# Performance work log

Hardware: AMD Instinct MI355X
Metric: run time of the kernel (lower is better)

Reference implementation:

```python
import jax, jax.numpy as jnp
import numpy as np

B, SQ, ST, SI = 8, 4096, 77, 16
C, DC, H = 1280, 2048, 20
DH = C // H  # 64
SCALE = 1.0 / np.sqrt(DH).astype(np.float32)
SCALE_ID = 1.0
SCALE_HAIR = 1.0


def setup_inputs() -> dict:
    key = jax.random.key(0)
    ks = jax.random.split(key, 12)
    std = 0.02
    return {
        "hidden_states": jax.random.normal(ks[0], (B, SQ, C), jnp.float32),
        "text_states": jax.random.normal(ks[1], (B, ST, DC), jnp.float32),
        "id_states": jax.random.normal(ks[2], (B, SI, DC), jnp.float32),
        "hair_states": jax.random.normal(ks[3], (B, SI, DC), jnp.float32),
        # weights stored as [in, out] (transpose of torch nn.Linear layout)
        "Wq": jax.random.normal(ks[4], (C, C), jnp.float32) * std,
        "Wk": jax.random.normal(ks[5], (DC, C), jnp.float32) * std,
        "Wv": jax.random.normal(ks[6], (DC, C), jnp.float32) * std,
        "Wo": jax.random.normal(ks[7], (C, C), jnp.float32) * std,
        "b_o": jnp.zeros((C,), jnp.float32),
        "Wk_id": jax.random.normal(ks[8], (DC, C), jnp.float32) * std,
        "Wv_id": jax.random.normal(ks[9], (DC, C), jnp.float32) * std,
        "Wk_hair": jax.random.normal(ks[10], (DC, C), jnp.float32) * std,
        "Wv_hair": jax.random.normal(ks[11], (DC, C), jnp.float32) * std,
    }


def _heads(x):
    # [B, S, C] -> [B, H, S, DH]
    b, s, _ = x.shape
    return x.reshape(b, s, H, DH).transpose(0, 2, 1, 3)


def _merge(x):
    # [B, H, S, DH] -> [B, S, C]
    b, h, s, d = x.shape
    return x.transpose(0, 2, 1, 3).reshape(b, s, h * d)


def _attend(q, k, v):
    # q: [B,H,Sq,DH], k/v: [B,H,Sk,DH]; fp32 scores (attn_fp32=True)
    scores = jnp.einsum("bhqd,bhkd->bhqk", q.astype(jnp.float32), k.astype(jnp.float32)) * SCALE
    p = jax.nn.softmax(scores, axis=-1)
    return jnp.einsum("bhqk,bhkd->bhqd", p, v.astype(jnp.float32))


def reference(hidden_states, text_states, id_states, hair_states, Wq, Wk, Wv, Wo, b_o, Wk_id, Wv_id, Wk_hair, Wv_hair):
    q = _heads(hidden_states @ Wq)
    # base cross-attention to text (standard diffusers AttnProcessor)
    base = _attend(q, _heads(text_states @ Wk), _heads(text_states @ Wv))
    result = _merge(base) @ Wo + b_o
    # ID branch: own K/V projections, shared query and to_out
    out_id = _attend(q, _heads(id_states @ Wk_id), _heads(id_states @ Wv_id))
    result = result + SCALE_ID * (_merge(out_id) @ Wo + b_o)
    # hair branch
    out_h = _attend(q, _heads(hair_states @ Wk_hair), _heads(hair_states @ Wv_hair))
    result = result + SCALE_HAIR * (_merge(out_h) @ Wo + b_o)
    return result
```

## Files before the change

### kernel.cpp

```cpp
#include <hip/hip_runtime.h>
#include <cstdint>
#include <cstddef>

typedef unsigned short u16;
typedef __attribute__((ext_vector_type(4))) float     f32x4_t;
typedef __attribute__((ext_vector_type(8))) __bf16    bf16x8_t;
typedef __attribute__((ext_vector_type(8))) u16       u16x8_t;
typedef __attribute__((ext_vector_type(4))) u16       u16x4_t;
typedef __attribute__((ext_vector_type(4))) float     fvec4_t;

#define DEVI __device__ __forceinline__

constexpr int Bn  = 8;
constexpr int SQn = 4096;
constexpr int STn = 77;
constexpr int SIn = 16;
constexpr int Cn  = 1280;
constexpr int DCn = 2048;
constexpr int Hn  = 20;
constexpr float SCALEf = 0.125f;
constexpr float L2E    = 1.4426950408889634f;

typedef const __attribute__((address_space(1))) void* gas_t;
typedef __attribute__((address_space(3))) void*       las_t;

DEVI u16 f2bf(float f) {
  union { float f; unsigned u; } cv; cv.f = f;
  unsigned u = cv.u;
  return (u16)((u + 0x7FFFu + ((u >> 16) & 1u)) >> 16);
}

__global__ __launch_bounds__(256) void cast_bf16_kernel(
    const float* __restrict__ src, u16* __restrict__ dst, int n8) {
  int i = blockIdx.x * 256 + threadIdx.x;
  if (i >= n8) return;
  const fvec4_t* s4 = (const fvec4_t*)src;
  fvec4_t a = s4[2 * i], b = s4[2 * i + 1];
  u16x8_t o;
  o[0] = f2bf(a[0]); o[1] = f2bf(a[1]); o[2] = f2bf(a[2]); o[3] = f2bf(a[3]);
  o[4] = f2bf(b[0]); o[5] = f2bf(b[1]); o[6] = f2bf(b[2]); o[7] = f2bf(b[3]);
  ((u16x8_t*)dst)[i] = o;
}

struct TrArgs {
  const float* src[8];
  u16*         dst[8];
  int          Kd[8];
};

__global__ __launch_bounds__(256) void transpose_cast_kernel(TrArgs ta) {
  int z = blockIdx.z;
  int K = ta.Kd[z];
  int k0 = blockIdx.x * 32;
  if (k0 >= K) return;
  int n0 = blockIdx.y * 32;
  __shared__ float tile[32][33];
  int tx = threadIdx.x & 31, ty = threadIdx.x >> 5;
  const float* src = ta.src[z];
#pragma unroll
  for (int i = 0; i < 4; i++) {
    int r = ty + 8 * i;
    tile[r][tx] = src[(size_t)(k0 + r) * Cn + n0 + tx];
  }
  __syncthreads();
  u16* dst = ta.dst[z];
#pragma unroll
  for (int i = 0; i < 4; i++) {
    int r = ty + 8 * i;
    dst[(size_t)(n0 + r) * K + k0 + tx] = f2bf(tile[tx][r]);
  }
}

template <int OUT_MODE, int A_HM>
__global__ __launch_bounds__(512, 2) void gemm256_kernel(
    const u16* __restrict__ A, const u16* __restrict__ Bt,
    void* __restrict__ Cout, const float* __restrict__ bias, int M, int K) {
  __shared__ __align__(16) u16 lds[2][2][256 * 64];
  const int t = threadIdx.x;
  const int w = t >> 6, l = t & 63;
  const int wr = w >> 2, wc = w & 3;
  const int lr = l & 15;
  const int m0 = blockIdx.x * 256, n0 = blockIdx.y * 256;
  const int NT = K >> 6;

  f32x4_t acc[8][4];
#pragma unroll
  for (int am = 0; am < 8; am++)
#pragma unroll
    for (int an = 0; an < 4; an++) {
      f32x4_t z = {0.f, 0.f, 0.f, 0.f};
      acc[am][an] = z;
    }

  auto stagePart = [&](int cb, int kt, int i) {
    const int k0 = kt * 64;
    int row = i * 64 + w * 8 + (l >> 3);
    int col16 = (l & 7) ^ (row & 7);
    const u16* ga;
    if (A_HM) {
      int gr = m0 + row, bb = gr >> 12, ss = gr & 4095;
      ga = A + (((size_t)bb * Hn + kt) * SQn + ss) * 64 + col16 * 8;
    } else {
      ga = A + (size_t)(m0 + row) * K + k0 + col16 * 8;
    }
    __builtin_amdgcn_global_load_lds((gas_t)ga, (las_t)(&lds[cb][0][0] + (size_t)(i * 512 + w * 64) * 8), 16, 0, 0);
    const u16* gb = Bt + (size_t)(n0 + row) * K + k0 + col16 * 8;
    __builtin_amdgcn_global_load_lds((gas_t)gb, (las_t)(&lds[cb][1][0] + (size_t)(i * 512 + w * 64) * 8), 16, 0, 0);
  };
  auto readA8 = [&](bf16x8_t (&dst)[8], const u16* bA, int kh) {
#pragma unroll
    for (int m = 0; m < 8; m++) {
      int row = wr * 128 + m * 16 + lr;
      int slot = kh * 4 + (l >> 4);
      dst[m] = *(const bf16x8_t*)&bA[row * 64 + ((slot ^ (row & 7)) * 8)];
    }
  };
  auto readB4 = [&](bf16x8_t (&dst)[4], const u16* bB, int kh) {
#pragma unroll
    for (int n = 0; n < 4; n++) {
      int row = wc * 64 + n * 16 + lr;
      int slot = kh * 4 + (l >> 4);
      dst[n] = *(const bf16x8_t*)&bB[row * 64 + ((slot ^ (row & 7)) * 8)];
    }
  };
  auto mfma32 = [&](bf16x8_t (&Af)[8], bf16x8_t (&Bf)[4]) {
    __builtin_amdgcn_s_setprio(1);
#pragma unroll
    for (int m = 0; m < 8; m++)
#pragma unroll
      for (int n = 0; n < 4; n++)
        acc[m][n] = __builtin_amdgcn_mfma_f32_16x16x32_bf16(Af[m], Bf[n], acc[m][n], 0, 0, 0);
    __builtin_amdgcn_s_setprio(0);
  };

#pragma unroll
  for (int i = 0; i < 4; i++) stagePart(0, 0, i);
#pragma unroll
  for (int i = 0; i < 4; i++) stagePart(1, 1, i);
  asm volatile("s_waitcnt vmcnt(8)" ::: "memory");
  __builtin_amdgcn_sched_barrier(0);
  __builtin_amdgcn_s_barrier();

  for (int kt = 0; kt < NT; kt++) {
    const int cb = kt & 1;
    const u16* bA = &lds[cb][0][0];
    const u16* bB = &lds[cb][1][0];
    const bool st = (kt + 2 < NT);
    bf16x8_t Af[8], Bf[4];

    readA8(Af, bA, 0);
    readB4(Bf, bB, 0);
    asm volatile("s_waitcnt lgkmcnt(0)" ::: "memory");
    __builtin_amdgcn_sched_barrier(0);
    mfma32(Af, Bf);

    readA8(Af, bA, 1);
    readB4(Bf, bB, 1);
    __builtin_amdgcn_s_barrier();
    if (st) {
      stagePart(cb, kt + 2, 0); stagePart(cb, kt + 2, 1);
      stagePart(cb, kt + 2, 2); stagePart(cb, kt + 2, 3);
    }
    asm volatile("s_waitcnt lgkmcnt(0)" ::: "memory");
    __builtin_amdgcn_sched_barrier(0);
    mfma32(Af, Bf);

    if (st) {
      asm volatile("s_waitcnt vmcnt(8)" ::: "memory");
    } else if (kt + 1 < NT) {
      asm volatile("s_waitcnt vmcnt(0)" ::: "memory");
    }
    __builtin_amdgcn_sched_barrier(0);
    __builtin_amdgcn_s_barrier();
  }

#pragma unroll
  for (int am = 0; am < 8; am++) {
    int rbase = m0 + wr * 128 + am * 16 + (l >> 4) * 4;
#pragma unroll
    for (int an = 0; an < 4; an++) {
      int col = n0 + wc * 64 + an * 16 + lr;
#pragma unroll
      for (int j = 0; j < 4; j++) {
        int r = rbase + j;
        if (OUT_MODE == 1) {
          ((float*)Cout)[(size_t)r * Cn + col] = acc[am][an][j] + 3.0f * bias[col];
        } else {
          int bb = r >> 12, ss = r & 4095;
          int hh = (n0 >> 6) + wc, dd = an * 16 + lr;
          ((u16*)Cout)[(((size_t)bb * Hn + hh) * SQn + ss) * 64 + dd] = f2bf(acc[am][an][j]);
        }
      }
    }
  }
}

DEVI void gemm_body(const u16* __restrict__ A, const u16* __restrict__ Bt,
                    u16* __restrict__ Cout, int M, int S, int K, int mtile, int ntile) {
  __shared__ __align__(16) u16 lA[128 * 64];
  __shared__ __align__(16) u16 lB[128 * 64];
  const int t = threadIdx.x;
  const int w = t >> 6, l = t & 63;
  const int wr = w >> 1, wc = w & 1;
  const int m0 = mtile * 128, n0 = ntile * 128;
  const int lr = l & 15, lk = (l >> 4) * 8;

  f32x4_t acc[4][4];
#pragma unroll
  for (int m = 0; m < 4; m++)
#pragma unroll
    for (int n = 0; n < 4; n++) {
      f32x4_t z = {0.f, 0.f, 0.f, 0.f};
      acc[m][n] = z;
    }

  for (int k0 = 0; k0 < K; k0 += 64) {
    __syncthreads();
#pragma unroll
    for (int i = 0; i < 4; i++) {
      int c = i * 256 + t;
      int row = c >> 3, ch = c & 7;
      int rA = m0 + row;
      rA = rA < M ? rA : M - 1;
      const u16* ga = A + (size_t)rA * K + k0 + ch * 8;
      __builtin_amdgcn_global_load_lds((gas_t)ga, (las_t)&lA[(i * 256 + w * 64) * 8], 16, 0, 0);
      const u16* gb = Bt + (size_t)(n0 + row) * K + k0 + ch * 8;
      __builtin_amdgcn_global_load_lds((gas_t)gb, (las_t)&lB[(i * 256 + w * 64) * 8], 16, 0, 0);
    }
    __syncthreads();
#pragma unroll
    for (int kk = 0; kk < 2; kk++) {
      bf16x8_t af[4], bf[4];
#pragma unroll
      for (int m = 0; m < 4; m++)
        af[m] = *(const bf16x8_t*)&lA[(64 * wr + 16 * m + lr) * 64 + kk * 32 + lk];
#pragma unroll
      for (int n = 0; n < 4; n++)
        bf[n] = *(const bf16x8_t*)&lB[(64 * wc + 16 * n + lr) * 64 + kk * 32 + lk];
#pragma unroll
      for (int m = 0; m < 4; m++)
#pragma unroll
        for (int n = 0; n < 4; n++)
          acc[m][n] = __builtin_amdgcn_mfma_f32_16x16x32_bf16(af[m], bf[n], acc[m][n], 0, 0, 0);
    }
  }

  const int rj = (l >> 4) * 4;
  const int hh = ntile * 2 + wc;
#pragma unroll
  for (int m = 0; m < 4; m++) {
    int rbase = m0 + 64 * wr + 16 * m + rj;
#pragma unroll
    for (int n = 0; n < 4; n++) {
      int dd = 16 * n + lr;
#pragma unroll
      for (int j = 0; j < 4; j++) {
        int r = rbase + j;
        if (r < M) {
          int bb = r / S, ss = r - bb * S;
          Cout[(((size_t)bb * Hn + hh) * S + ss) * 64 + dd] = f2bf(acc[m][n][j]);
        }
      }
    }
  }
}

struct KV6 {
  const u16* A[6];
  const u16* Bt[6];
  u16*       Cp[6];
  int        M[6];
  int        S[6];
};

__global__ __launch_bounds__(256) void gemm_kv_kernel(KV6 kv) {
  int z = blockIdx.z;
  int M = kv.M[z];
  if ((int)blockIdx.x * 128 >= M) return;
  gemm_body(kv.A[z], kv.Bt[z], kv.Cp[z], M, kv.S[z], DCn, blockIdx.x, blockIdx.y);
}

__global__ __launch_bounds__(256) void attn_kernel(
    const u16* __restrict__ q,
    const u16* __restrict__ ktx, const u16* __restrict__ vtx,
    const u16* __restrict__ kid, const u16* __restrict__ vid,
    const u16* __restrict__ kh,  const u16* __restrict__ vh,
    u16* __restrict__ osum) {
  __shared__ __align__(16) u16 KP[4 * 16 * 136];
  __shared__ __align__(16) u16 Vt[64 * 128];

  const int t = threadIdx.x, w = t >> 6, l = t & 63;
  const int bh = blockIdx.y;
  const int lr = l & 15, lk = (l >> 4) * 8;

  const u16* qB   = q   + ((size_t)bh) * SQn * 64;
  const u16* ktxB = ktx + ((size_t)bh) * STn * 64;
  const u16* vtxB = vtx + ((size_t)bh) * STn * 64;
  const u16* kidB = kid + ((size_t)bh) * SIn * 64;
  const u16* vidB = vid + ((size_t)bh) * SIn * 64;
  const u16* khB  = kh  + ((size_t)bh) * SIn * 64;
  const u16* vhB  = vh  + ((size_t)bh) * SIn * 64;
  u16*       oB   = osum + ((size_t)bh) * SQn * 64;

  for (int i = t; i < 112 * 8; i += 256) {
    int row = i >> 3, ch = i & 7;
    u16x8_t vv;
#pragma unroll
    for (int x = 0; x < 8; x++) vv[x] = 0;
    if (row < 77)
      vv = *(const u16x8_t*)(ktxB + (size_t)row * 64 + ch * 8);
    else if (row >= 80 && row < 96)
      vv = *(const u16x8_t*)(kidB + (size_t)(row - 80) * 64 + ch * 8);
    else if (row >= 96)
      vv = *(const u16x8_t*)(khB + (size_t)(row - 96) * 64 + ch * 8);
    *(u16x8_t*)&KP[row * 72 + ch * 8] = vv;
  }
  for (int i = t; i < 128 * 8; i += 256) {
    int key = i >> 3, ch = i & 7;
    u16x8_t vv;
#pragma unroll
    for (int x = 0; x < 8; x++) vv[x] = 0;
    if (key < 77)
      vv = *(const u16x8_t*)(vtxB + (size_t)key * 64 + ch * 8);
    else if (key >= 80 && key < 96)
      vv = *(const u16x8_t*)(vidB + (size_t)(key - 80) * 64 + ch * 8);
    else if (key >= 96 && key < 112)
      vv = *(const u16x8_t*)(vhB + (size_t)(key - 96) * 64 + ch * 8);
    int G = key >> 3, wk = key & 7;
#pragma unroll
    for (int x = 0; x < 8; x++) {
      int d = ch * 8 + x;
      int Gs = G ^ x ^ ch;
      Vt[d * 128 + Gs * 8 + wk] = vv[x];
    }
  }
  __syncthreads();

  bf16x8_t kf[7][2];
#pragma unroll
  for (int tt = 0; tt < 7; tt++)
#pragma unroll
    for (int kk = 0; kk < 2; kk++)
      kf[tt][kk] = *(const bf16x8_t*)&KP[(tt * 16 + lr) * 72 + kk * 32 + lk];
  __syncthreads();

  u16* Pw = &KP[w * 16 * 136];
  {
    u16x4_t z4; z4[0] = 0; z4[1] = 0; z4[2] = 0; z4[3] = 0;
    *(u16x4_t*)&Pw[(l >> 2) * 136 + 112 + (l & 3) * 4] = z4;
  }

  for (int rt = 0; rt < 4; rt++) {
    const int s0 = blockIdx.x * 256 + w * 64 + rt * 16;
    bf16x8_t qf[2];
#pragma unroll
    for (int kk = 0; kk < 2; kk++)
      qf[kk] = *(const bf16x8_t*)&qB[(size_t)(s0 + lr) * 64 + kk * 32 + lk];

    f32x4_t sc[7];
#pragma unroll
    for (int tt = 0; tt < 7; tt++) {
      f32x4_t z = {0.f, 0.f, 0.f, 0.f};
      z = __builtin_amdgcn_mfma_f32_16x16x32_bf16(qf[0], kf[tt][0], z, 0, 0, 0);
      z = __builtin_amdgcn_mfma_f32_16x16x32_bf16(qf[1], kf[tt][1], z, 0, 0, 0);
      sc[tt] = z;
    }
#pragma unroll
    for (int tt = 0; tt < 7; tt++)
#pragma unroll
      for (int j = 0; j < 4; j++) sc[tt][j] *= SCALEf;
    if (lr >= 13) {
#pragma unroll
      for (int j = 0; j < 4; j++) sc[4][j] = -3.0e38f;
    }

    float mx[4], sm[4], inv[4];

#pragma unroll
    for (int j = 0; j < 4; j++) {
      float m = sc[0][j];
      m = fmaxf(m, sc[1][j]); m = fmaxf(m, sc[2][j]);
      m = fmaxf(m, sc[3][j]); m = fmaxf(m, sc[4][j]);
      mx[j] = m;
    }
#pragma unroll
    for (int d = 1; d < 16; d <<= 1)
#pragma unroll
      for (int j = 0; j < 4; j++) mx[j] = fmaxf(mx[j], __shfl_xor(mx[j], d));
#pragma unroll
    for (int j = 0; j < 4; j++) sm[j] = 0.f;
#pragma unroll
    for (int tt = 0; tt < 5; tt++)
#pragma unroll
      for (int j = 0; j < 4; j++) {
        float p = __builtin_amdgcn_exp2f((sc[tt][j] - mx[j]) * L2E);
        sc[tt][j] = p;
        sm[j] += p;
      }
#pragma unroll
    for (int d = 1; d < 16; d <<= 1)
#pragma unroll
      for (int j = 0; j < 4; j++) sm[j] += __shfl_xor(sm[j], d);
#pragma unroll
    for (int j = 0; j < 4; j++) inv[j] = __builtin_amdgcn_rcpf(sm[j]);
#pragma unroll
    for (int tt = 0; tt < 5; tt++)
#pragma unroll
      for (int j = 0; j < 4; j++) {
        __bf16 pb = (__bf16)(sc[tt][j] * inv[j]);
        Pw[((l >> 4) * 4 + j) * 136 + tt * 16 + lr] = *(u16*)&pb;
      }

#pragma unroll
    for (int j = 0; j < 4; j++) mx[j] = sc[5][j];
#pragma unroll
    for (int d = 1; d < 16; d <<= 1)
#pragma unroll
      for (int j = 0; j < 4; j++) mx[j] = fmaxf(mx[j], __shfl_xor(mx[j], d));
#pragma unroll
    for (int j = 0; j < 4; j++) {
      float p = __builtin_amdgcn_exp2f((sc[5][j] - mx[j]) * L2E);
      sc[5][j] = p;
      sm[j] = p;
    }
#pragma unroll
    for (int d = 1; d < 16; d <<= 1)
#pragma unroll
      for (int j = 0; j < 4; j++) sm[j] += __shfl_xor(sm[j], d);
#pragma unroll
    for (int j = 0; j < 4; j++) {
      __bf16 pb = (__bf16)(sc[5][j] * __builtin_amdgcn_rcpf(sm[j]));
      Pw[((l >> 4) * 4 + j) * 136 + 80 + lr] = *(u16*)&pb;
    }

#pragma unroll
    for (int j = 0; j < 4; j++) mx[j] = sc[6][j];
#pragma unroll
    for (int d = 1; d < 16; d <<= 1)
#pragma unroll
      for (int j = 0; j < 4; j++) mx[j] = fmaxf(mx[j], __shfl_xor(mx[j], d));
#pragma unroll
    for (int j = 0; j < 4; j++) {
      float p = __builtin_amdgcn_exp2f((sc[6][j] - mx[j]) * L2E);
      sc[6][j] = p;
      sm[j] = p;
    }
#pragma unroll
    for (int d = 1; d < 16; d <<= 1)
#pragma unroll
      for (int j = 0; j < 4; j++) sm[j] += __shfl_xor(sm[j], d);
#pragma unroll
    for (int j = 0; j < 4; j++) {
      __bf16 pb = (__bf16)(sc[6][j] * __builtin_amdgcn_rcpf(sm[j]));
      Pw[((l >> 4) * 4 + j) * 136 + 96 + lr] = *(u16*)&pb;
    }

    f32x4_t oacc[4];
#pragma unroll
    for (int n = 0; n < 4; n++) {
      f32x4_t z = {0.f, 0.f, 0.f, 0.f};
      oacc[n] = z;
    }
#pragma unroll
    for (int ktile = 0; ktile < 4; ktile++) {
      bf16x8_t pf = *(const bf16x8_t*)&Pw[lr * 136 + ktile * 32 + lk];
#pragma unroll
      for (int n = 0; n < 4; n++) {
        int d = 16 * n + lr;
        int Gs = (4 * ktile + (l >> 4)) ^ (d & 7) ^ ((d >> 3) & 7);
        bf16x8_t vf = *(const bf16x8_t*)&Vt[d * 128 + Gs * 8];
        oacc[n] = __builtin_amdgcn_mfma_f32_16x16x32_bf16(pf, vf, oacc[n], 0, 0, 0);
      }
    }
#pragma unroll
    for (int n = 0; n < 4; n++)
#pragma unroll
      for (int j = 0; j < 4; j++) {
        int srow = s0 + (l >> 4) * 4 + j;
        __bf16 ob = (__bf16)oacc[n][j];
        oB[(size_t)srow * 64 + 16 * n + lr] = *(u16*)&ob;
      }
  }
}

extern "C" void kernel_launch(void* const* d_in, const int* in_sizes, int n_in,
                              void* d_out, int out_size, void* d_ws, size_t ws_size,
                              hipStream_t stream) {
  (void)in_sizes; (void)n_in; (void)out_size; (void)ws_size;
  const float* hidden  = (const float*)d_in[0];
  const float* text    = (const float*)d_in[1];
  const float* ids     = (const float*)d_in[2];
  const float* hair    = (const float*)d_in[3];
  const float* Wq      = (const float*)d_in[4];
  const float* Wk      = (const float*)d_in[5];
  const float* Wv      = (const float*)d_in[6];
  const float* Wo      = (const float*)d_in[7];
  const float* b_o     = (const float*)d_in[8];
  const float* Wk_id   = (const float*)d_in[9];
  const float* Wv_id   = (const float*)d_in[10];
  const float* Wk_hair = (const float*)d_in[11];
  const float* Wv_hair = (const float*)d_in[12];
  float* out = (float*)d_out;

  char* ws = (char*)d_ws;
  size_t off = 0;
  auto carve = [&](size_t bytes) -> char* {
    char* p = ws + off;
    off += (bytes + 255) & ~(size_t)255;
    return p;
  };

  u16* h_bf    = (u16*)carve((size_t)Bn * SQn * Cn * 2);
  u16* q_bf    = (u16*)carve((size_t)Bn * SQn * Cn * 2);
  u16* text_bf = (u16*)carve((size_t)Bn * STn * DCn * 2);
  u16* id_bf   = (u16*)carve((size_t)Bn * SIn * DCn * 2);
  u16* hair_bf = (u16*)carve((size_t)Bn * SIn * DCn * 2);
  u16* Wq_t    = (u16*)carve((size_t)Cn * Cn * 2);
  u16* Wo_t    = (u16*)carve((size_t)Cn * Cn * 2);
  u16* Wk_t    = (u16*)carve((size_t)DCn * Cn * 2);
  u16* Wv_t    = (u16*)carve((size_t)DCn * Cn * 2);
  u16* Wkid_t  = (u16*)carve((size_t)DCn * Cn * 2);
  u16* Wvid_t  = (u16*)carve((size_t)DCn * Cn * 2);
  u16* Wkh_t   = (u16*)carve((size_t)DCn * Cn * 2);
  u16* Wvh_t   = (u16*)carve((size_t)DCn * Cn * 2);
  u16* k_text  = (u16*)carve((size_t)Bn * STn * Cn * 2);
  u16* v_text  = (u16*)carve((size_t)Bn * STn * Cn * 2);
  u16* k_id    = (u16*)carve((size_t)Bn * SIn * Cn * 2);
  u16* v_id    = (u16*)carve((size_t)Bn * SIn * Cn * 2);
  u16* k_hr    = (u16*)carve((size_t)Bn * SIn * Cn * 2);
  u16* v_hr    = (u16*)carve((size_t)Bn * SIn * Cn * 2);
  u16* attn_sum = h_bf;

  {
    int n8 = Bn * SQn * Cn / 8;
    cast_bf16_kernel<<<dim3((n8 + 255) / 256), 256, 0, stream>>>(hidden, h_bf, n8);
  }
  {
    int n8 = Bn * STn * DCn / 8;
    cast_bf16_kernel<<<dim3((n8 + 255) / 256), 256, 0, stream>>>(text, text_bf, n8);
  }
  {
    int n8 = Bn * SIn * DCn / 8;
    cast_bf16_kernel<<<dim3((n8 + 255) / 256), 256, 0, stream>>>(ids, id_bf, n8);
    cast_bf16_kernel<<<dim3((n8 + 255) / 256), 256, 0, stream>>>(hair, hair_bf, n8);
  }

  {
    TrArgs ta;
    ta.src[0] = Wq;      ta.dst[0] = Wq_t;   ta.Kd[0] = Cn;
    ta.src[1] = Wo;      ta.dst[1] = Wo_t;   ta.Kd[1] = Cn;
    ta.src[2] = Wk;      ta.dst[2] = Wk_t;   ta.Kd[2] = DCn;
    ta.src[3] = Wv;      ta.dst[3] = Wv_t;   ta.Kd[3] = DCn;
    ta.src[4] = Wk_id;   ta.dst[4] = Wkid_t; ta.Kd[4] = DCn;
    ta.src[5] = Wv_id;   ta.dst[5] = Wvid_t; ta.Kd[5] = DCn;
    ta.src[6] = Wk_hair; ta.dst[6] = Wkh_t;  ta.Kd[6] = DCn;
    ta.src[7] = Wv_hair; ta.dst[7] = Wvh_t;  ta.Kd[7] = DCn;
    transpose_cast_kernel<<<dim3(DCn / 32, Cn / 32, 8), 256, 0, stream>>>(ta);
  }

  gemm256_kernel<2, 0><<<dim3(Bn * SQn / 256, Cn / 256), 512, 0, stream>>>(
      h_bf, Wq_t, q_bf, nullptr, Bn * SQn, Cn);

  {
    KV6 kv;
    kv.A[0] = text_bf; kv.Bt[0] = Wk_t;   kv.Cp[0] = k_text; kv.M[0] = Bn * STn; kv.S[0] = STn;
    kv.A[1] = text_bf; kv.Bt[1] = Wv_t;   kv.Cp[1] = v_text; kv.M[1] = Bn * STn; kv.S[1] = STn;
    kv.A[2] = id_bf;   kv.Bt[2] = Wkid_t; kv.Cp[2] = k_id;   kv.M[2] = Bn * SIn; kv.S[2] = SIn;
    kv.A[3] = id_bf;   kv.Bt[3] = Wvid_t; kv.Cp[3] = v_id;   kv.M[3] = Bn * SIn; kv.S[3] = SIn;
    kv.A[4] = hair_bf; kv.Bt[4] = Wkh_t;  kv.Cp[4] = k_hr;   kv.M[4] = Bn * SIn; kv.S[4] = SIn;
    kv.A[5] = hair_bf; kv.Bt[5] = Wvh_t;  kv.Cp[5] = v_hr;   kv.M[5] = Bn * SIn; kv.S[5] = SIn;
    gemm_kv_kernel<<<dim3((Bn * STn + 127) / 128, Cn / 128, 6), 256, 0, stream>>>(kv);
  }

  attn_kernel<<<dim3(SQn / 256, Bn * Hn), 256, 0, stream>>>(
      q_bf, k_text, v_text, k_id, v_id, k_hr, v_hr, attn_sum);

  gemm256_kernel<1, 1><<<dim3(Bn * SQn / 256, Cn / 256), 512, 0, stream>>>(
      attn_sum, Wo_t, out, b_o, Bn * SQn, Cn);
}
```

Baseline: 482.4 us.

## Software-pipeline LDS fragment reads with MFMAs and stage bf16 epilogue through LDS

The GEMM main loop now double-buffers the register fragments. The next half-K's LDS reads are issued before the current MFMA block, so LDS latency overlaps with matrix math instead of stalling before each MFMA group. For the head-major bf16 output mode, the epilogue writes accumulators into a padded, swizzled LDS region per wave and then emits 16-byte coalesced global stores, replacing scattered 2-byte writes. This raises LDS allocation for that mode and register pressure from holding two fragment sets, which could hurt occupancy at 2 blocks per CU.

Result: no change. 480.8 us (-0.3%).

```diff
diff --git a/kernel.cpp b/kernel.cpp
--- a/kernel.cpp
+++ b/kernel.cpp
@@ -75,7 +75,7 @@
 __global__ __launch_bounds__(512, 2) void gemm256_kernel(
     const u16* __restrict__ A, const u16* __restrict__ Bt,
     void* __restrict__ Cout, const float* __restrict__ bias, int M, int K) {
-  __shared__ __align__(16) u16 lds[2][2][256 * 64];
+  __shared__ __align__(16) u16 lds[(OUT_MODE == 2) ? 73728 : 65536];
   const int t = threadIdx.x;
   const int w = t >> 6, l = t & 63;
   const int wr = w >> 2, wc = w & 3;
@@ -83,6 +83,8 @@
   const int m0 = blockIdx.x * 256, n0 = blockIdx.y * 256;
   const int NT = K >> 6;
 
+  auto bufp = [&](int cb, int op) -> u16* { return lds + (size_t)(cb * 2 + op) * 16384; };
+
   f32x4_t acc[8][4];
 #pragma unroll
   for (int am = 0; am < 8; am++)
@@ -92,20 +94,23 @@
       acc[am][an] = z;
     }
 
-  auto stagePart = [&](int cb, int kt, int i) {
+  auto stageAll = [&](int cb, int kt) {
     const int k0 = kt * 64;
-    int row = i * 64 + w * 8 + (l >> 3);
-    int col16 = (l & 7) ^ (row & 7);
-    const u16* ga;
-    if (A_HM) {
-      int gr = m0 + row, bb = gr >> 12, ss = gr & 4095;
-      ga = A + (((size_t)bb * Hn + kt) * SQn + ss) * 64 + col16 * 8;
-    } else {
-      ga = A + (size_t)(m0 + row) * K + k0 + col16 * 8;
-    }
-    __builtin_amdgcn_global_load_lds((gas_t)ga, (las_t)(&lds[cb][0][0] + (size_t)(i * 512 + w * 64) * 8), 16, 0, 0);
-    const u16* gb = Bt + (size_t)(n0 + row) * K + k0 + col16 * 8;
-    __builtin_amdgcn_global_load_lds((gas_t)gb, (las_t)(&lds[cb][1][0] + (size_t)(i * 512 + w * 64) * 8), 16, 0, 0);
+#pragma unroll
+    for (int i = 0; i < 4; i++) {
+      int row = i * 64 + w * 8 + (l >> 3);
+      int col16 = (l & 7) ^ (row & 7);
+      const u16* ga;
+      if (A_HM) {
+        int gr = m0 + row, bb = gr >> 12, ss = gr & 4095;
+        ga = A + (((size_t)bb * Hn + kt) * SQn + ss) * 64 + col16 * 8;
+      } else {
+        ga = A + (size_t)(m0 + row) * K + k0 + col16 * 8;
+      }
+      __builtin_amdgcn_global_load_lds((gas_t)ga, (las_t)(bufp(cb, 0) + (size_t)(i * 512 + w * 64) * 8), 16, 0, 0);
+      const u16* gb = Bt + (size_t)(n0 + row) * K + k0 + col16 * 8;
+      __builtin_amdgcn_global_load_lds((gas_t)gb, (las_t)(bufp(cb, 1) + (size_t)(i * 512 + w * 64) * 8), 16, 0, 0);
+    }
   };
   auto readA8 = [&](bf16x8_t (&dst)[8], const u16* bA, int kh) {
 #pragma unroll
@@ -133,37 +138,30 @@
     __builtin_amdgcn_s_setprio(0);
   };
 
-#pragma unroll
-  for (int i = 0; i < 4; i++) stagePart(0, 0, i);
-#pragma unroll
-  for (int i = 0; i < 4; i++) stagePart(1, 1, i);
+  stageAll(0, 0);
+  stageAll(1, 1);
   asm volatile("s_waitcnt vmcnt(8)" ::: "memory");
   __builtin_amdgcn_sched_barrier(0);
   __builtin_amdgcn_s_barrier();
 
+  bf16x8_t Af0[8], Bf0[4], Af1[8], Bf1[4];
+  readA8(Af0, bufp(0, 0), 0);
+  readB4(Bf0, bufp(0, 1), 0);
+  asm volatile("s_waitcnt lgkmcnt(0)" ::: "memory");
+  __builtin_amdgcn_sched_barrier(0);
+
   for (int kt = 0; kt < NT; kt++) {
     const int cb = kt & 1;
-    const u16* bA = &lds[cb][0][0];
-    const u16* bB = &lds[cb][1][0];
     const bool st = (kt + 2 < NT);
-    bf16x8_t Af[8], Bf[4];
-
-    readA8(Af, bA, 0);
-    readB4(Bf, bB, 0);
+
+    readA8(Af1, bufp(cb, 0), 1);
+    readB4(Bf1, bufp(cb, 1), 1);
+    __builtin_amdgcn_sched_barrier(0);
+    __builtin_amdgcn_s_barrier();
+    if (st) stageAll(cb, kt + 2);
+    mfma32(Af0, Bf0);
     asm volatile("s_waitcnt lgkmcnt(0)" ::: "memory");
     __builtin_amdgcn_sched_barrier(0);
-    mfma32(Af, Bf);
-
-    readA8(Af, bA, 1);
-    readB4(Bf, bB, 1);
-    __builtin_amdgcn_s_barrier();
-    if (st) {
-      stagePart(cb, kt + 2, 0); stagePart(cb, kt + 2, 1);
-      stagePart(cb, kt + 2, 2); stagePart(cb, kt + 2, 3);
-    }
-    asm volatile("s_waitcnt lgkmcnt(0)" ::: "memory");
-    __builtin_amdgcn_sched_barrier(0);
-    mfma32(Af, Bf);
 
     if (st) {
       asm volatile("s_waitcnt vmcnt(8)" ::: "memory");
@@ -172,25 +170,57 @@
     }
     __builtin_amdgcn_sched_barrier(0);
     __builtin_amdgcn_s_barrier();
-  }
-
-#pragma unroll
-  for (int am = 0; am < 8; am++) {
-    int rbase = m0 + wr * 128 + am * 16 + (l >> 4) * 4;
-#pragma unroll
-    for (int an = 0; an < 4; an++) {
-      int col = n0 + wc * 64 + an * 16 + lr;
-#pragma unroll
-      for (int j = 0; j < 4; j++) {
-        int r = rbase + j;
-        if (OUT_MODE == 1) {
+
+    if (kt + 1 < NT) {
+      readA8(Af0, bufp(cb ^ 1, 0), 0);
+      readB4(Bf0, bufp(cb ^ 1, 1), 0);
+      __builtin_amdgcn_sched_barrier(0);
+    }
+    mfma32(Af1, Bf1);
+    asm volatile("s_waitcnt lgkmcnt(0)" ::: "memory");
+    __builtin_amdgcn_sched_barrier(0);
+  }
+
+  if (OUT_MODE == 1) {
+#pragma unroll
+    for (int am = 0; am < 8; am++) {
+      int rbase = m0 + wr * 128 + am * 16 + (l >> 4) * 4;
+#pragma unroll
+      for (int an = 0; an < 4; an++) {
+        int col = n0 + wc * 64 + an * 16 + lr;
+#pragma unroll
+        for (int j = 0; j < 4; j++) {
+          int r = rbase + j;
           ((float*)Cout)[(size_t)r * Cn + col] = acc[am][an][j] + 3.0f * bias[col];
-        } else {
-          int bb = r >> 12, ss = r & 4095;
-          int hh = (n0 >> 6) + wc, dd = an * 16 + lr;
-          ((u16*)Cout)[(((size_t)bb * Hn + hh) * SQn + ss) * 64 + dd] = f2bf(acc[am][an][j]);
         }
       }
+    }
+  } else {
+    __syncthreads();
+    u16* R = lds + (size_t)w * 9216;
+#pragma unroll
+    for (int am = 0; am < 8; am++)
+#pragma unroll
+      for (int an = 0; an < 4; an++)
+#pragma unroll
+        for (int j = 0; j < 4; j++) {
+          int row = am * 16 + (l >> 4) * 4 + j;
+          int g = an * 2 + (lr >> 3);
+          int gp = g ^ (row & 7);
+          R[row * 72 + gp * 8 + (lr & 7)] = f2bf(acc[am][an][j]);
+        }
+    const int hh = (n0 >> 6) + wc;
+    const int rbase = m0 + wr * 128;
+    const int bb = rbase >> 12;
+    const int ssb = rbase & 4095;
+    u16* dstW = (u16*)Cout + (((size_t)bb * Hn + hh) * SQn + ssb) * 64;
+#pragma unroll
+    for (int it = 0; it < 16; it++) {
+      int rr = it * 8 + (l >> 3);
+      int gr = l & 7;
+      int gp = gr ^ (rr & 7);
+      u16x8_t v = *(const u16x8_t*)&R[rr * 72 + gp * 8];
+      *(u16x8_t*)&dstW[(size_t)rr * 64 + gr * 8] = v;
     }
   }
 }
```

## Replace double-buffered LDS prefetch pipeline with single-buffer synchronous staging in GEMM

Applied to the files above, without the earlier changes.

Removes the two-stage LDS double buffering from the 256x256 GEMM kernel. Each K-tile is now loaded into a single LDS buffer, the kernel waits for all loads and synchronises, then computes. This halves LDS use per block, which may allow more resident blocks. In exchange, global-load latency is no longer overlapped with MFMA work inside a block.

Result: slower. 561.9 us (+16.5%).

```diff
diff --git a/kernel.cpp b/kernel.cpp
--- a/kernel.cpp
+++ b/kernel.cpp
@@ -75,7 +75,7 @@
 __global__ __launch_bounds__(512, 2) void gemm256_kernel(
     const u16* __restrict__ A, const u16* __restrict__ Bt,
     void* __restrict__ Cout, const float* __restrict__ bias, int M, int K) {
-  __shared__ __align__(16) u16 lds[2][2][256 * 64];
+  __shared__ __align__(16) u16 lds[2][256 * 64];
   const int t = threadIdx.x;
   const int w = t >> 6, l = t & 63;
   const int wr = w >> 2, wc = w & 3;
@@ -92,35 +92,38 @@
       acc[am][an] = z;
     }
 
-  auto stagePart = [&](int cb, int kt, int i) {
+  auto stageAll = [&](int kt) {
     const int k0 = kt * 64;
-    int row = i * 64 + w * 8 + (l >> 3);
-    int col16 = (l & 7) ^ (row & 7);
-    const u16* ga;
-    if (A_HM) {
-      int gr = m0 + row, bb = gr >> 12, ss = gr & 4095;
-      ga = A + (((size_t)bb * Hn + kt) * SQn + ss) * 64 + col16 * 8;
-    } else {
-      ga = A + (size_t)(m0 + row) * K + k0 + col16 * 8;
-    }
-    __builtin_amdgcn_global_load_lds((gas_t)ga, (las_t)(&lds[cb][0][0] + (size_t)(i * 512 + w * 64) * 8), 16, 0, 0);
-    const u16* gb = Bt + (size_t)(n0 + row) * K + k0 + col16 * 8;
-    __builtin_amdgcn_global_load_lds((gas_t)gb, (las_t)(&lds[cb][1][0] + (size_t)(i * 512 + w * 64) * 8), 16, 0, 0);
+#pragma unroll
+    for (int i = 0; i < 4; i++) {
+      int row = i * 64 + w * 8 + (l >> 3);
+      int col16 = (l & 7) ^ (row & 7);
+      const u16* ga;
+      if (A_HM) {
+        int gr = m0 + row, bb = gr >> 12, ss = gr & 4095;
+        ga = A + (((size_t)bb * Hn + kt) * SQn + ss) * 64 + col16 * 8;
+      } else {
+        ga = A + (size_t)(m0 + row) * K + k0 + col16 * 8;
+      }
+      __builtin_amdgcn_global_load_lds((gas_t)ga, (las_t)(&lds[0][0] + (size_t)(i * 512 + w * 64) * 8), 16, 0, 0);
+      const u16* gb = Bt + (size_t)(n0 + row) * K + k0 + col16 * 8;
+      __builtin_amdgcn_global_load_lds((gas_t)gb, (las_t)(&lds[1][0] + (size_t)(i * 512 + w * 64) * 8), 16, 0, 0);
+    }
   };
-  auto readA8 = [&](bf16x8_t (&dst)[8], const u16* bA, int kh) {
+  auto readA8 = [&](bf16x8_t (&dst)[8], int kh) {
 #pragma unroll
     for (int m = 0; m < 8; m++) {
       int row = wr * 128 + m * 16 + lr;
       int slot = kh * 4 + (l >> 4);
-      dst[m] = *(const bf16x8_t*)&bA[row * 64 + ((slot ^ (row & 7)) * 8)];
+      dst[m] = *(const bf16x8_t*)&lds[0][row * 64 + ((slot ^ (row & 7)) * 8)];
     }
   };
-  auto readB4 = [&](bf16x8_t (&dst)[4], const u16* bB, int kh) {
+  auto readB4 = [&](bf16x8_t (&dst)[4], int kh) {
 #pragma unroll
     for (int n = 0; n < 4; n++) {
       int row = wc * 64 + n * 16 + lr;
       int slot = kh * 4 + (l >> 4);
-      dst[n] = *(const bf16x8_t*)&bB[row * 64 + ((slot ^ (row & 7)) * 8)];
+      dst[n] = *(const bf16x8_t*)&lds[1][row * 64 + ((slot ^ (row & 7)) * 8)];
     }
   };
   auto mfma32 = [&](bf16x8_t (&Af)[8], bf16x8_t (&Bf)[4]) {
@@ -133,45 +136,24 @@
     __builtin_amdgcn_s_setprio(0);
   };
 
-#pragma unroll
-  for (int i = 0; i < 4; i++) stagePart(0, 0, i);
-#pragma unroll
-  for (int i = 0; i < 4; i++) stagePart(1, 1, i);
-  asm volatile("s_waitcnt vmcnt(8)" ::: "memory");
-  __builtin_amdgcn_sched_barrier(0);
-  __builtin_amdgcn_s_barrier();
-
   for (int kt = 0; kt < NT; kt++) {
-    const int cb = kt & 1;
-    const u16* bA = &lds[cb][0][0];
-    const u16* bB = &lds[cb][1][0];
-    const bool st = (kt + 2 < NT);
+    __builtin_amdgcn_s_barrier();
+    stageAll(kt);
+    asm volatile("s_waitcnt vmcnt(0)" ::: "memory");
+    __builtin_amdgcn_sched_barrier(0);
+    __builtin_amdgcn_s_barrier();
+
     bf16x8_t Af[8], Bf[4];
-
-    readA8(Af, bA, 0);
-    readB4(Bf, bB, 0);
+    readA8(Af, 0);
+    readB4(Bf, 0);
     asm volatile("s_waitcnt lgkmcnt(0)" ::: "memory");
     __builtin_amdgcn_sched_barrier(0);
     mfma32(Af, Bf);
-
-    readA8(Af, bA, 1);
-    readB4(Bf, bB, 1);
-    __builtin_amdgcn_s_barrier();
-    if (st) {
-      stagePart(cb, kt + 2, 0); stagePart(cb, kt + 2, 1);
-      stagePart(cb, kt + 2, 2); stagePart(cb, kt + 2, 3);
-    }
+    readA8(Af, 1);
+    readB4(Bf, 1);
     asm volatile("s_waitcnt lgkmcnt(0)" ::: "memory");
     __builtin_amdgcn_sched_barrier(0);
     mfma32(Af, Bf);
-
-    if (st) {
-      asm volatile("s_waitcnt vmcnt(8)" ::: "memory");
-    } else if (kt + 1 < NT) {
-      asm volatile("s_waitcnt vmcnt(0)" ::: "memory");
-    }
-    __builtin_amdgcn_sched_barrier(0);
-    __builtin_amdgcn_s_barrier();
   }
 
 #pragma unroll
```
